# Performance work log

Hardware: AMD Instinct MI355X
Metric: run time of the kernel (lower is better)

The kernel has to match this reference:

```python
import jax, jax.numpy as jnp
import numpy as np
import math

B, S, D, H, L, FF = 16, 512, 1024, 16, 4, 4096
DK = D // H
EPS = 1e-5
NEG = -1e32


def make_pe(max_len, d_model):
    pos = np.arange(max_len, dtype=np.float32)[:, None]
    div = np.exp(np.arange(0, d_model, 2, dtype=np.float32) * (-math.log(10000.0) / d_model))
    pe = np.zeros((max_len, d_model), dtype=np.float32)
    pe[:, 0::2] = np.sin(pos * div)
    pe[:, 1::2] = np.cos(pos * div)
    return jnp.asarray(pe[None])  # [1, max_len, d_model]


def setup_inputs() -> dict:
    key = jax.random.key(0)
    ks = jax.random.split(key, 32)
    sd = 0.02
    inp = {
        'q_embed_data': jax.random.normal(ks[0], (B, S, D), jnp.float32),
        'qa_embed_data': jax.random.normal(ks[1], (B, S, D), jnp.float32),
        'forget_rate': jax.random.uniform(ks[2], (B, 1, S, 1), jnp.float32),
        'pe': make_pe(S, D),
        'Wk': jax.random.normal(ks[3], (L, D, D), jnp.float32) * sd,
        'bk': jnp.zeros((L, D), jnp.float32),
        'Wv': jax.random.normal(ks[4], (L, D, D), jnp.float32) * sd,
        'bv': jnp.zeros((L, D), jnp.float32),
        'Wo': jax.random.normal(ks[5], (L, D, D), jnp.float32) * sd,
        'bo': jnp.zeros((L, D), jnp.float32),
        'W1': jax.random.normal(ks[6], (L, D, FF), jnp.float32) * sd,
        'b1': jnp.zeros((L, FF), jnp.float32),
        'W2': jax.random.normal(ks[7], (L, FF, D), jnp.float32) * sd,
        'b2': jnp.zeros((L, D), jnp.float32),
        'ln1_g': jnp.ones((L, D), jnp.float32),
        'ln1_b': jnp.zeros((L, D), jnp.float32),
        'ln2_g': jnp.ones((L, D), jnp.float32),
        'ln2_b': jnp.zeros((L, D), jnp.float32),
    }
    return inp


def layernorm(x, g, b):
    m = jnp.mean(x, -1, keepdims=True)
    v = jnp.mean((x - m) ** 2, -1, keepdims=True)
    return (x - m) * jax.lax.rsqrt(v + EPS) * g + b


def forward(q_embed_data, qa_embed_data, forget_rate, pe,
            Wk, bk, Wv, bv, Wo, bo, W1, b1, W2, b2,
            ln1_g, ln1_b, ln2_g, ln2_b):
    x = q_embed_data + pe[:, :S]
    y = qa_embed_data + pe[:, :S]
    # mask==0 path: allowed positions are strictly below diagonal (j < i)
    allowed = jnp.tril(jnp.ones((S, S), bool), k=-1)
    scale = 1.0 / math.sqrt(DK)
    for l in range(L):
        # kq_same: q also uses k_linear
        k = (x @ Wk[l] + bk[l]).reshape(B, S, H, DK).transpose(0, 2, 1, 3)
        q = k
        v = (y @ Wv[l] + bv[l]).reshape(B, S, H, DK).transpose(0, 2, 1, 3)
        scores = jnp.einsum('bhid,bhjd->bhij', q, k) * scale
        scores = scores * forget_rate  # [B,1,S,1] broadcasts over heads/cols
        scores = jnp.where(allowed, scores, NEG)
        attn = jax.nn.softmax(scores, axis=-1)
        attn = attn.at[:, :, 0, :].set(0.0)  # zero_pad of first query row
        out = jnp.einsum('bhij,bhjd->bhid', attn, v)
        out = out.transpose(0, 2, 1, 3).reshape(B, S, D) @ Wo[l] + bo[l]
        x = layernorm(x + out, ln1_g[l], ln1_b[l])
        ff = jax.nn.relu(x @ W1[l] + b1[l]) @ W2[l] + b2[l]
        x = layernorm(x + ff, ln2_g[l], ln2_b[l])
    return x


def reference(q_embed_data, qa_embed_data, forget_rate, pe,
              Wk, bk, Wv, bv, Wo, bo, W1, b1, W2, b2,
              ln1_g, ln1_b, ln2_g, ln2_b):
    return forward(q_embed_data, qa_embed_data, forget_rate, pe,
                   Wk, bk, Wv, bv, Wo, bo, W1, b1, W2, b2,
                   ln1_g, ln1_b, ln2_g, ln2_b)
```

## Files before the change

### kernel.cpp

```cpp
#include <hip/hip_runtime.h>
#include <hip/hip_bf16.h>
#include <cstdint>
#include <cstddef>

#define Bq 16
#define Sq 512
#define Dq 1024
#define Hq 16
#define Lq 4
#define FFq 4096
#define Mq (Bq * Sq)

typedef unsigned short ushort_t;
typedef __attribute__((ext_vector_type(8))) short short8;
typedef __attribute__((ext_vector_type(8))) unsigned short ushortx8;
typedef __attribute__((ext_vector_type(4))) unsigned short ushortx4;
typedef __attribute__((ext_vector_type(4))) float floatx4;

__device__ __forceinline__ float bf2f(ushort_t u) {
  union { unsigned int i; float f; } x;
  x.i = ((unsigned int)u) << 16;
  return x.f;
}
__device__ __forceinline__ ushort_t f2bf(float f) {
  unsigned int u = __float_as_uint(f);
  u += 0x7fffu + ((u >> 16) & 1u);
  return (ushort_t)(u >> 16);
}

#define GLL16(gp, lp) __builtin_amdgcn_global_load_lds( \
    (__attribute__((address_space(1))) void*)(gp),      \
    (__attribute__((address_space(3))) void*)(lp), 16, 0, 0)

__global__ void probe_kernel(const ushort_t* __restrict__ pe,
                             const ushort_t* __restrict__ g1,
                             int* __restrict__ flags)
{
  if (threadIdx.x == 0 && blockIdx.x == 0) {
    flags[0] = (pe[1] == (ushort_t)0x3F80u) ? 1 : 0;
    flags[1] = (g1[0] == (ushort_t)0x3F80u) ? 1 : 0;
  }
}

struct CvtArgs {
  const void* src[10];
  ushort_t*   dst[10];
  int         n[10];
  int         fi[10];
  int         cum[11];
};
__global__ __launch_bounds__(256) void convert_all_kernel(
    CvtArgs a, const int* __restrict__ flags)
{
  const int bidx = blockIdx.x;
  int s = 0;
  while (s < 9 && bidx >= a.cum[s + 1]) ++s;
  const int i = (bidx - a.cum[s]) * 256 + threadIdx.x;
  if (i >= a.n[s]) return;
  if (flags[a.fi[s]]) a.dst[s][i] = ((const ushort_t*)a.src[s])[i];
  else                a.dst[s][i] = f2bf(((const float*)a.src[s])[i]);
}

__global__ __launch_bounds__(256) void gemm_bt_kernel(
    const ushort_t* __restrict__ A, const ushort_t* __restrict__ BT,
    const ushort_t* __restrict__ bias, ushort_t* __restrict__ C,
    int N, int K, int relu)
{
  __shared__ __align__(16) ushort_t As[2][128 * 32];
  __shared__ __align__(16) ushort_t Bs[2][128 * 32];

  const int t = threadIdx.x;
  const int lane = t & 63;
  const int w = t >> 6;
  const int la = lane & 15;
  const int lb = lane >> 4;

  int bx = blockIdx.x, by = blockIdx.y;
  {
    const int gx = gridDim.x, gy = gridDim.y;
    if ((gy & 7) == 0) {
      const int orig = by * gx + bx;
      const int xcd = orig & 7;
      const int local = orig >> 3;
      const int rows = gy >> 3;
      const int mi = local % rows;
      const int ni = local / rows;
      by = xcd * rows + mi;
      bx = ni;
    }
  }
  const long m0 = (long)by * 128;
  const long n0 = (long)bx * 128;
  const int nk = K >> 5;

  const int r0 = t >> 2;
  const int c0 = (t & 3) << 3;
  const ushort_t* gA = A + (m0 + r0) * K + c0;
  const ushort_t* gB = BT + (n0 + r0) * K + c0;
  const long rowoff = (long)64 * K;
  const int lo0 = (w * 64) * 8;
  const int lo1 = (w * 64 + 256) * 8;

  const floatx4 z4 = {0.f, 0.f, 0.f, 0.f};
  floatx4 acc[4][4];
#pragma unroll
  for (int i = 0; i < 4; ++i)
#pragma unroll
    for (int j = 0; j < 4; ++j) acc[i][j] = z4;

  GLL16(gA, &As[0][lo0]);
  GLL16(gA + rowoff, &As[0][lo1]);
  GLL16(gB, &Bs[0][lo0]);
  GLL16(gB + rowoff, &Bs[0][lo1]);
  __syncthreads();

  const int wm = (w >> 1) * 64;
  const int wn = (w & 1) * 64;
  int cur = 0;

  for (int kt = 1; kt < nk; ++kt) {
    const long ko = (long)kt * 32;
    GLL16(gA + ko, &As[cur ^ 1][lo0]);
    GLL16(gA + rowoff + ko, &As[cur ^ 1][lo1]);
    GLL16(gB + ko, &Bs[cur ^ 1][lo0]);
    GLL16(gB + rowoff + ko, &Bs[cur ^ 1][lo1]);

    short8 af[4], bfr[4];
#pragma unroll
    for (int mf = 0; mf < 4; ++mf)
      af[mf] = *(const short8*)&As[cur][(wm + mf * 16 + la) * 32 + lb * 8];
#pragma unroll
    for (int nf = 0; nf < 4; ++nf)
      bfr[nf] = *(const short8*)&Bs[cur][(wn + nf * 16 + la) * 32 + lb * 8];
#pragma unroll
    for (int mf = 0; mf < 4; ++mf)
#pragma unroll
      for (int nf = 0; nf < 4; ++nf)
        acc[mf][nf] = __builtin_amdgcn_mfma_f32_16x16x32_bf16(af[mf], bfr[nf], acc[mf][nf], 0, 0, 0);

    __syncthreads();
    cur ^= 1;
  }
  {
    short8 af[4], bfr[4];
#pragma unroll
    for (int mf = 0; mf < 4; ++mf)
      af[mf] = *(const short8*)&As[cur][(wm + mf * 16 + la) * 32 + lb * 8];
#pragma unroll
    for (int nf = 0; nf < 4; ++nf)
      bfr[nf] = *(const short8*)&Bs[cur][(wn + nf * 16 + la) * 32 + lb * 8];
#pragma unroll
    for (int mf = 0; mf < 4; ++mf)
#pragma unroll
      for (int nf = 0; nf < 4; ++nf)
        acc[mf][nf] = __builtin_amdgcn_mfma_f32_16x16x32_bf16(af[mf], bfr[nf], acc[mf][nf], 0, 0, 0);
  }

#pragma unroll
  for (int nf = 0; nf < 4; ++nf) {
    const long col = n0 + wn + nf * 16 + la;
    const float bsv = bf2f(bias[col]);
#pragma unroll
    for (int mf = 0; mf < 4; ++mf) {
      const long row = m0 + wm + mf * 16 + lb * 4;
      ushort_t* cp = C + row * N + col;
      const floatx4 v = acc[mf][nf];
#pragma unroll
      for (int r = 0; r < 4; ++r) {
        float x = v[r] + bsv;
        if (relu) x = fmaxf(x, 0.0f);
        cp[(long)r * N] = f2bf(x);
      }
    }
  }
}

__global__ __launch_bounds__(256) void attn_kernel(
    const ushort_t* __restrict__ kq, const ushort_t* __restrict__ vt,
    const ushort_t* __restrict__ fr, ushort_t* __restrict__ ao)
{
  __shared__ __align__(16) ushort_t P[4][64 * 72];
  const int t = threadIdx.x;
  const int lane = t & 63;
  const int w4 = t >> 6;
  const int wq = blockIdx.y * 4 + w4;
  const int b = blockIdx.x >> 4;
  const int h = blockIdx.x & 15;
  const int la = lane & 15;
  const int lb = lane >> 4;
  const int i0 = wq * 64;
  const long kbase = ((long)b * Sq) * Dq + h * 64;
  const long vbase = ((long)(b * Hq + h)) * (64L * Sq);

  short8 qf[4][2];
#pragma unroll
  for (int mf = 0; mf < 4; ++mf)
#pragma unroll
    for (int tt = 0; tt < 2; ++tt)
      qf[mf][tt] = *(const short8*)&kq[kbase + (long)(i0 + mf * 16 + la) * Dq + tt * 32 + lb * 8];

  float frs[4][4];
#pragma unroll
  for (int mf = 0; mf < 4; ++mf)
#pragma unroll
    for (int r = 0; r < 4; ++r)
      frs[mf][r] = 0.125f * bf2f(fr[b * Sq + i0 + mf * 16 + lb * 4 + r]);

  const floatx4 z4 = {0.f, 0.f, 0.f, 0.f};
  floatx4 o[4][4];
  float mrun[4][4], lrun[4][4];
#pragma unroll
  for (int mf = 0; mf < 4; ++mf)
#pragma unroll
    for (int x = 0; x < 4; ++x) {
      o[mf][x] = z4;
      mrun[mf][x] = -1e30f;
      lrun[mf][x] = 0.0f;
    }

  for (int jt = 0; jt <= wq; ++jt) {
    const int j0 = jt * 64;
    floatx4 s[4][4];
#pragma unroll
    for (int mf = 0; mf < 4; ++mf)
#pragma unroll
      for (int jf = 0; jf < 4; ++jf) s[mf][jf] = z4;

#pragma unroll
    for (int tt = 0; tt < 2; ++tt) {
      short8 kf[4];
#pragma unroll
      for (int jf = 0; jf < 4; ++jf)
        kf[jf] = *(const short8*)&kq[kbase + (long)(j0 + jf * 16 + la) * Dq + tt * 32 + lb * 8];
#pragma unroll
      for (int mf = 0; mf < 4; ++mf)
#pragma unroll
        for (int jf = 0; jf < 4; ++jf)
          s[mf][jf] = __builtin_amdgcn_mfma_f32_16x16x32_bf16(qf[mf][tt], kf[jf], s[mf][jf], 0, 0, 0);
    }

    const bool diag = (jt == wq);
#pragma unroll
    for (int mf = 0; mf < 4; ++mf)
#pragma unroll
      for (int jf = 0; jf < 4; ++jf)
#pragma unroll
        for (int r = 0; r < 4; ++r) {
          float x = s[mf][jf][r] * frs[mf][r];
          if (diag && (j0 + jf * 16 + la) >= (i0 + mf * 16 + lb * 4 + r)) x = -1e30f;
          s[mf][jf][r] = x;
        }

#pragma unroll
    for (int mf = 0; mf < 4; ++mf)
#pragma unroll
      for (int r = 0; r < 4; ++r) {
        float pm = fmaxf(fmaxf(s[mf][0][r], s[mf][1][r]), fmaxf(s[mf][2][r], s[mf][3][r]));
        pm = fmaxf(pm, __shfl_xor(pm, 1));
        pm = fmaxf(pm, __shfl_xor(pm, 2));
        pm = fmaxf(pm, __shfl_xor(pm, 4));
        pm = fmaxf(pm, __shfl_xor(pm, 8));
        const float mo = mrun[mf][r];
        const float mn = fmaxf(mo, pm);
        const float sc = __expf(mo - mn);
        mrun[mf][r] = mn;
        float rs = 0.0f;
#pragma unroll
        for (int jf = 0; jf < 4; ++jf) {
          const float p = __expf(s[mf][jf][r] - mn);
          s[mf][jf][r] = p;
          rs += p;
        }
        rs += __shfl_xor(rs, 1);
        rs += __shfl_xor(rs, 2);
        rs += __shfl_xor(rs, 4);
        rs += __shfl_xor(rs, 8);
        lrun[mf][r] = lrun[mf][r] * sc + rs;
#pragma unroll
        for (int df = 0; df < 4; ++df) o[mf][df][r] *= sc;
      }

#pragma unroll
    for (int mf = 0; mf < 4; ++mf)
#pragma unroll
      for (int jf = 0; jf < 4; ++jf)
#pragma unroll
        for (int r = 0; r < 4; ++r)
          P[w4][(mf * 16 + lb * 4 + r) * 72 + jf * 16 + la] = f2bf(s[mf][jf][r]);

#pragma unroll
    for (int tt = 0; tt < 2; ++tt) {
      short8 pf[4], vf[4];
#pragma unroll
      for (int mf = 0; mf < 4; ++mf)
        pf[mf] = *(const short8*)&P[w4][(mf * 16 + la) * 72 + tt * 32 + lb * 8];
#pragma unroll
      for (int df = 0; df < 4; ++df)
        vf[df] = *(const short8*)&vt[vbase + (long)(df * 16 + la) * Sq + j0 + tt * 32 + lb * 8];
#pragma unroll
      for (int mf = 0; mf < 4; ++mf)
#pragma unroll
        for (int df = 0; df < 4; ++df)
          o[mf][df] = __builtin_amdgcn_mfma_f32_16x16x32_bf16(pf[mf], vf[df], o[mf][df], 0, 0, 0);
    }
  }

#pragma unroll
  for (int mf = 0; mf < 4; ++mf)
#pragma unroll
    for (int df = 0; df < 4; ++df)
#pragma unroll
      for (int r = 0; r < 4; ++r) {
        const int ii = i0 + mf * 16 + lb * 4 + r;
        const float vv = (ii == 0) ? 0.0f : o[mf][df][r] / lrun[mf][r];
        ao[((long)b * Sq + ii) * Dq + h * 64 + df * 16 + la] = f2bf(vv);
      }
}

__global__ __launch_bounds__(256) void ln_kernel(
    float* __restrict__ xf, const ushort_t* __restrict__ add,
    const ushort_t* __restrict__ g, const ushort_t* __restrict__ bb,
    ushort_t* __restrict__ outb, float* __restrict__ outf,
    const int* __restrict__ flags, int final_)
{
  __shared__ float red[2][4];
  const long row = blockIdx.x;
  const int t = threadIdx.x;
  const int c = t * 4;
  float* xr = xf + row * Dq;
  const ushort_t* ar = add + row * Dq;

  floatx4 xv = *(floatx4*)&xr[c];
  ushortx4 av = *(const ushortx4*)&ar[c];
  float v[4];
  float s1 = 0.f, s2 = 0.f;
#pragma unroll
  for (int e = 0; e < 4; ++e) {
    v[e] = xv[e] + bf2f(av[e]);
    s1 += v[e];
    s2 += v[e] * v[e];
  }
#pragma unroll
  for (int m = 1; m < 64; m <<= 1) {
    s1 += __shfl_xor(s1, m);
    s2 += __shfl_xor(s2, m);
  }
  const int lane = t & 63, w = t >> 6;
  if (lane == 0) { red[0][w] = s1; red[1][w] = s2; }
  __syncthreads();
  s1 = red[0][0] + red[0][1] + red[0][2] + red[0][3];
  s2 = red[1][0] + red[1][1] + red[1][2] + red[1][3];
  const float mean = s1 * (1.0f / Dq);
  const float var = fmaxf(s2 * (1.0f / Dq) - mean * mean, 0.0f);
  const float rstd = rsqrtf(var + 1e-5f);
  ushortx4 gv = *(const ushortx4*)&g[c];
  ushortx4 bv = *(const ushortx4*)&bb[c];
  ushortx4 ob;
  floatx4 xo;
#pragma unroll
  for (int e = 0; e < 4; ++e) {
    const float y = (v[e] - mean) * rstd * bf2f(gv[e]) + bf2f(bv[e]);
    xo[e] = y;
    ob[e] = f2bf(y);
  }
  *(floatx4*)&xr[c] = xo;
  if (final_ && !flags[0]) {
    *(floatx4*)&outf[row * Dq + c] = xo;
  } else {
    *(ushortx4*)&outb[row * Dq + c] = ob;
  }
}

__global__ __launch_bounds__(256) void addpe_kernel(
    const void* __restrict__ qe, const void* __restrict__ qa,
    const void* __restrict__ pe, float* __restrict__ xf,
    ushort_t* __restrict__ xb, ushort_t* __restrict__ yb,
    const int* __restrict__ flags)
{
  const long i = ((long)blockIdx.x * 256 + threadIdx.x) * 8;
  const long sd = i & ((long)Sq * Dq - 1);
  const bool isb = flags[0] != 0;
  float q[8], a[8], p[8];
  if (isb) {
    ushortx8 q8 = *(const ushortx8*)((const ushort_t*)qe + i);
    ushortx8 a8 = *(const ushortx8*)((const ushort_t*)qa + i);
    ushortx8 p8 = *(const ushortx8*)((const ushort_t*)pe + sd);
#pragma unroll
    for (int e = 0; e < 8; ++e) { q[e] = bf2f(q8[e]); a[e] = bf2f(a8[e]); p[e] = bf2f(p8[e]); }
  } else {
    const float* qp = (const float*)qe + i;
    const float* ap = (const float*)qa + i;
    const float* pp = (const float*)pe + sd;
    floatx4 q0 = *(const floatx4*)qp, q1 = *(const floatx4*)(qp + 4);
    floatx4 a0 = *(const floatx4*)ap, a1 = *(const floatx4*)(ap + 4);
    floatx4 p0 = *(const floatx4*)pp, p1 = *(const floatx4*)(pp + 4);
#pragma unroll
    for (int e = 0; e < 4; ++e) {
      q[e] = q0[e]; q[e + 4] = q1[e];
      a[e] = a0[e]; a[e + 4] = a1[e];
      p[e] = p0[e]; p[e + 4] = p1[e];
    }
  }
  ushortx8 xo, yo;
  floatx4 f0, f1;
#pragma unroll
  for (int e = 0; e < 8; ++e) {
    const float xvv = (isb ? q[e] : bf2f(f2bf(q[e]))) + (isb ? p[e] : bf2f(f2bf(p[e])));
    const float yvv = (isb ? a[e] : bf2f(f2bf(a[e]))) + (isb ? p[e] : bf2f(f2bf(p[e])));
    if (e < 4) { f0[e] = xvv; } else { f1[e - 4] = xvv; }
    xo[e] = f2bf(xvv);
    yo[e] = f2bf(yvv);
  }
  *(floatx4*)&xf[i] = f0;
  *(floatx4*)&xf[i + 4] = f1;
  *(ushortx8*)&xb[i] = xo;
  *(ushortx8*)&yb[i] = yo;
}

__global__ __launch_bounds__(256) void transpose_kernel(
    const void* __restrict__ src, ushort_t* __restrict__ dst, int K, int N,
    const int* __restrict__ flags)
{
  __shared__ __align__(16) ushort_t tile[64][72];
  const bool isb = flags[1] != 0;
  const long base = (long)blockIdx.z * K * N;
  const int k0 = blockIdx.y * 64, n0 = blockIdx.x * 64;
  const int t = threadIdx.x;
  const int r = t >> 3;
  const int cc = (t & 7) << 3;
#pragma unroll
  for (int it = 0; it < 2; ++it) {
    const int rr = r + it * 32;
    const long gi = base + (long)(k0 + rr) * N + n0 + cc;
    if (isb) {
      *(short8*)&tile[rr][cc] = *(const short8*)((const ushort_t*)src + gi);
    } else {
      const float* sf = (const float*)src + gi;
      floatx4 v0 = *(const floatx4*)sf;
      floatx4 v1 = *(const floatx4*)(sf + 4);
#pragma unroll
      for (int e = 0; e < 4; ++e) {
        tile[rr][cc + e] = f2bf(v0[e]);
        tile[rr][cc + 4 + e] = f2bf(v1[e]);
      }
    }
  }
  __syncthreads();
#pragma unroll
  for (int it = 0; it < 2; ++it) {
    const int rr = r + it * 32;
    short8 v;
#pragma unroll
    for (int e = 0; e < 8; ++e) v[e] = (short)tile[cc + e][rr];
    *(short8*)&dst[base + (long)(n0 + rr) * K + k0 + cc] = v;
  }
}

__global__ __launch_bounds__(256) void vtrans_kernel(
    const ushort_t* __restrict__ vb, ushort_t* __restrict__ vt)
{
  __shared__ __align__(16) ushort_t tile[64][72];
  const int b = blockIdx.y >> 4, h = blockIdx.y & 15;
  const int j0 = blockIdx.x * 64;
  const int t = threadIdx.x;
  const int r = t >> 3;
  const int cc = (t & 7) << 3;
#pragma unroll
  for (int it = 0; it < 2; ++it) {
    const int rr = r + it * 32;
    *(short8*)&tile[rr][cc] = *(const short8*)&vb[((long)b * Sq + j0 + rr) * Dq + h * 64 + cc];
  }
  __syncthreads();
#pragma unroll
  for (int it = 0; it < 2; ++it) {
    const int rr = r + it * 32;
    short8 v;
#pragma unroll
    for (int e = 0; e < 8; ++e) v[e] = (short)tile[cc + e][rr];
    *(short8*)&vt[((long)(b * Hq + h) * 64 + rr) * Sq + j0 + cc] = v;
  }
}

extern "C" void kernel_launch(void* const* d_in, const int* in_sizes, int n_in,
                              void* d_out, int out_size, void* d_ws, size_t ws_size,
                              hipStream_t stream)
{
  if (n_in < 18) return;
  const void* qe  = d_in[0];
  const void* qa  = d_in[1];
  const void* fr  = d_in[2];
  const void* pe  = d_in[3];
  const void* Wk  = d_in[4];
  const void* bk  = d_in[5];
  const void* Wv  = d_in[6];
  const void* bv  = d_in[7];
  const void* Wo  = d_in[8];
  const void* bo  = d_in[9];
  const void* W1  = d_in[10];
  const void* b1  = d_in[11];
  const void* W2  = d_in[12];
  const void* b2  = d_in[13];
  const void* g1  = d_in[14];
  const void* be1 = d_in[15];
  const void* g2  = d_in[16];
  const void* be2 = d_in[17];

  char* ws = (char*)d_ws;
  const size_t SM = 243269632L;
  const size_t NEED = SM + 114752L;
  if (ws_size < NEED) return;

  float*    xf   = (float*)   (ws + 0L);
  ushort_t* xb   = (ushort_t*)(ws + 33554432L);
  ushort_t* yb   = (ushort_t*)(ws + 50331648L);
  ushort_t* tmpD = (ushort_t*)(ws + 67108864L);
  ushort_t* WkT  = (ushort_t*)(ws + 83886080L);
  ushort_t* WvT  = (ushort_t*)(ws + 92274688L);
  ushort_t* WoT  = (ushort_t*)(ws + 100663296L);
  ushort_t* W1T  = (ushort_t*)(ws + 109051904L);
  ushort_t* W2T  = (ushort_t*)(ws + 142606336L);
  ushort_t* kb   = (ushort_t*)(ws + 176160768L);
  ushort_t* vbf  = (ushort_t*)(ws + 192937984L);
  ushort_t* vtb  = (ushort_t*)(ws + 209715200L);
  ushort_t* ff1  = kb;

  int*      flags = (int*)(ws + SM);
  ushort_t* frc  = (ushort_t*)(ws + SM + 64);
  ushort_t* bkc  = (ushort_t*)(ws + SM + 16448);
  ushort_t* bvc  = (ushort_t*)(ws + SM + 24640);
  ushort_t* boc  = (ushort_t*)(ws + SM + 32832);
  ushort_t* b1c  = (ushort_t*)(ws + SM + 41024);
  ushort_t* b2c  = (ushort_t*)(ws + SM + 73792);
  ushort_t* g1c  = (ushort_t*)(ws + SM + 81984);
  ushort_t* be1c = (ushort_t*)(ws + SM + 90176);
  ushort_t* g2c  = (ushort_t*)(ws + SM + 98368);
  ushort_t* be2c = (ushort_t*)(ws + SM + 106560);

  probe_kernel<<<1, 64, 0, stream>>>((const ushort_t*)pe, (const ushort_t*)g1, flags);

  {
    CvtArgs a;
    const void* srcs[10] = {fr, bk, bv, bo, b1, b2, g1, be1, g2, be2};
    ushort_t*   dsts[10] = {frc, bkc, bvc, boc, b1c, b2c, g1c, be1c, g2c, be2c};
    const int   ns[10]   = {8192, 4096, 4096, 4096, 16384, 4096, 4096, 4096, 4096, 4096};
    int cum = 0;
    for (int s = 0; s < 10; ++s) {
      a.src[s] = srcs[s]; a.dst[s] = dsts[s]; a.n[s] = ns[s];
      a.fi[s] = (s == 0) ? 0 : 1;
      a.cum[s] = cum;
      cum += (ns[s] + 255) / 256;
    }
    a.cum[10] = cum;
    convert_all_kernel<<<cum, 256, 0, stream>>>(a, flags);
  }

  transpose_kernel<<<dim3(16, 16, 4), 256, 0, stream>>>(Wk, WkT, 1024, 1024, flags);
  transpose_kernel<<<dim3(16, 16, 4), 256, 0, stream>>>(Wv, WvT, 1024, 1024, flags);
  transpose_kernel<<<dim3(16, 16, 4), 256, 0, stream>>>(Wo, WoT, 1024, 1024, flags);
  transpose_kernel<<<dim3(64, 16, 4), 256, 0, stream>>>(W1, W1T, 1024, 4096, flags);
  transpose_kernel<<<dim3(16, 64, 4), 256, 0, stream>>>(W2, W2T, 4096, 1024, flags);

  addpe_kernel<<<4096, 256, 0, stream>>>(qe, qa, pe, xf, xb, yb, flags);

  for (int l = 0; l < 4; ++l) {
    gemm_bt_kernel<<<dim3(8, 64), 256, 0, stream>>>(xb, WkT + (long)l * 1048576, bkc + l * 1024, kb, 1024, 1024, 0);
    gemm_bt_kernel<<<dim3(8, 64), 256, 0, stream>>>(yb, WvT + (long)l * 1048576, bvc + l * 1024, vbf, 1024, 1024, 0);
    vtrans_kernel<<<dim3(8, 256), 256, 0, stream>>>(vbf, vtb);
    attn_kernel<<<dim3(256, 2), 256, 0, stream>>>(kb, vtb, frc, vbf);
    gemm_bt_kernel<<<dim3(8, 64), 256, 0, stream>>>(vbf, WoT + (long)l * 1048576, boc + l * 1024, tmpD, 1024, 1024, 0);
    ln_kernel<<<8192, 256, 0, stream>>>(xf, tmpD, g1c + l * 1024, be1c + l * 1024, xb, nullptr, flags, 0);
    gemm_bt_kernel<<<dim3(32, 64), 256, 0, stream>>>(xb, W1T + (long)l * 4194304, b1c + l * 4096, ff1, 4096, 1024, 1);
    gemm_bt_kernel<<<dim3(8, 64), 256, 0, stream>>>(ff1, W2T + (long)l * 4194304, b2c + l * 1024, tmpD, 1024, 4096, 0);
    if (l == 3) {
      ln_kernel<<<8192, 256, 0, stream>>>(xf, tmpD, g2c + l * 1024, be2c + l * 1024,
                                          (ushort_t*)d_out, (float*)d_out, flags, 1);
    } else {
      ln_kernel<<<8192, 256, 0, stream>>>(xf, tmpD, g2c + l * 1024, be2c + l * 1024,
                                          xb, nullptr, flags, 0);
    }
  }
}
```

Measured before the change: 1.840 ms.

## Deepen GEMM pipeline to four LDS stages with XOR-swizzled layout

The GEMM main loop moves from a double buffer to a four-buffer LDS ring with three tiles prefetched ahead, and uses explicit vmcnt waits so loads for later tiles stay in flight while the current tile is computed. The LDS layout is also XOR-swizzled on the k-chunk index, in both the global-to-LDS placement and the fragment reads, to reduce bank conflicts. LDS use doubles to 64KB per block, which may lower occupancy. Correctness depends on the hand-counted vmcnt values matching the number of outstanding loads.

```diff
diff --git a/kernel.cpp b/kernel.cpp
--- a/kernel.cpp
+++ b/kernel.cpp
@@ -66,8 +66,8 @@
     const ushort_t* __restrict__ bias, ushort_t* __restrict__ C,
     int N, int K, int relu)
 {
-  __shared__ __align__(16) ushort_t As[2][128 * 32];
-  __shared__ __align__(16) ushort_t Bs[2][128 * 32];
+  __shared__ __align__(16) ushort_t As[4][4096];
+  __shared__ __align__(16) ushort_t Bs[4][4096];
 
   const int t = threadIdx.x;
   const int lane = t & 63;
@@ -83,23 +83,25 @@
       const int xcd = orig & 7;
       const int local = orig >> 3;
       const int rows = gy >> 3;
-      const int mi = local % rows;
-      const int ni = local / rows;
-      by = xcd * rows + mi;
-      bx = ni;
+      by = xcd * rows + local % rows;
+      bx = local / rows;
     }
   }
   const long m0 = (long)by * 128;
   const long n0 = (long)bx * 128;
   const int nk = K >> 5;
 
-  const int r0 = t >> 2;
-  const int c0 = (t & 3) << 3;
-  const ushort_t* gA = A + (m0 + r0) * K + c0;
-  const ushort_t* gB = BT + (n0 + r0) * K + c0;
-  const long rowoff = (long)64 * K;
-  const int lo0 = (w * 64) * 8;
-  const int lo1 = (w * 64 + 256) * 8;
+  const int f0 = (w << 7) + lane;
+  const int f1 = f0 + 64;
+  const int rA0 = f0 >> 2, rA1 = f1 >> 2;
+  const int kA0 = ((f0 & 3) ^ ((rA0 >> 1) & 3)) << 3;
+  const int kA1 = ((f1 & 3) ^ ((rA1 >> 1) & 3)) << 3;
+  const ushort_t* gA0 = A + (m0 + rA0) * K + kA0;
+  const ushort_t* gA1 = A + (m0 + rA1) * K + kA1;
+  const ushort_t* gB0 = BT + (n0 + rA0) * K + kA0;
+  const ushort_t* gB1 = BT + (n0 + rA1) * K + kA1;
+  const int lo0 = (w * 2 + 0) * 512;
+  const int lo1 = (w * 2 + 1) * 512;
 
   const floatx4 z4 = {0.f, 0.f, 0.f, 0.f};
   floatx4 acc[4][4];
@@ -108,53 +110,51 @@
 #pragma unroll
     for (int j = 0; j < 4; ++j) acc[i][j] = z4;
 
-  GLL16(gA, &As[0][lo0]);
-  GLL16(gA + rowoff, &As[0][lo1]);
-  GLL16(gB, &Bs[0][lo0]);
-  GLL16(gB + rowoff, &Bs[0][lo1]);
-  __syncthreads();
+#define STAGE(buf, kt) do {                      \
+    const long ko_ = (long)(kt) << 5;            \
+    GLL16(gA0 + ko_, &As[(buf)][lo0]);           \
+    GLL16(gA1 + ko_, &As[(buf)][lo1]);           \
+    GLL16(gB0 + ko_, &Bs[(buf)][lo0]);           \
+    GLL16(gB1 + ko_, &Bs[(buf)][lo1]);           \
+  } while (0)
+
+  STAGE(0, 0);
+  STAGE(1, 1);
+  STAGE(2, 2);
 
   const int wm = (w >> 1) * 64;
   const int wn = (w & 1) * 64;
-  int cur = 0;
-
-  for (int kt = 1; kt < nk; ++kt) {
-    const long ko = (long)kt * 32;
-    GLL16(gA + ko, &As[cur ^ 1][lo0]);
-    GLL16(gA + rowoff + ko, &As[cur ^ 1][lo1]);
-    GLL16(gB + ko, &Bs[cur ^ 1][lo0]);
-    GLL16(gB + rowoff + ko, &Bs[cur ^ 1][lo1]);
-
+
+  for (int kt = 0; kt < nk; ++kt) {
+    const int rem = nk - 1 - kt;
+    if (rem >= 2)      asm volatile("s_waitcnt vmcnt(8)" ::: "memory");
+    else if (rem == 1) asm volatile("s_waitcnt vmcnt(4)" ::: "memory");
+    else               asm volatile("s_waitcnt vmcnt(0)" ::: "memory");
+    __builtin_amdgcn_s_barrier();
+
+    const int cur = kt & 3;
     short8 af[4], bfr[4];
 #pragma unroll
-    for (int mf = 0; mf < 4; ++mf)
-      af[mf] = *(const short8*)&As[cur][(wm + mf * 16 + la) * 32 + lb * 8];
-#pragma unroll
-    for (int nf = 0; nf < 4; ++nf)
-      bfr[nf] = *(const short8*)&Bs[cur][(wn + nf * 16 + la) * 32 + lb * 8];
+    for (int mf = 0; mf < 4; ++mf) {
+      const int r = wm + mf * 16 + la;
+      af[mf] = *(const short8*)&As[cur][r * 32 + ((lb ^ ((r >> 1) & 3)) << 3)];
+    }
+#pragma unroll
+    for (int nf = 0; nf < 4; ++nf) {
+      const int r = wn + nf * 16 + la;
+      bfr[nf] = *(const short8*)&Bs[cur][r * 32 + ((lb ^ ((r >> 1) & 3)) << 3)];
+    }
 #pragma unroll
     for (int mf = 0; mf < 4; ++mf)
 #pragma unroll
       for (int nf = 0; nf < 4; ++nf)
         acc[mf][nf] = __builtin_amdgcn_mfma_f32_16x16x32_bf16(af[mf], bfr[nf], acc[mf][nf], 0, 0, 0);
 
-    __syncthreads();
-    cur ^= 1;
-  }
-  {
-    short8 af[4], bfr[4];
-#pragma unroll
-    for (int mf = 0; mf < 4; ++mf)
-      af[mf] = *(const short8*)&As[cur][(wm + mf * 16 + la) * 32 + lb * 8];
-#pragma unroll
-    for (int nf = 0; nf < 4; ++nf)
-      bfr[nf] = *(const short8*)&Bs[cur][(wn + nf * 16 + la) * 32 + lb * 8];
-#pragma unroll
-    for (int mf = 0; mf < 4; ++mf)
-#pragma unroll
-      for (int nf = 0; nf < 4; ++nf)
-        acc[mf][nf] = __builtin_amdgcn_mfma_f32_16x16x32_bf16(af[mf], bfr[nf], acc[mf][nf], 0, 0, 0);
-  }
+    asm volatile("s_waitcnt lgkmcnt(0)" ::: "memory");
+    __builtin_amdgcn_s_barrier();
+    if (kt + 3 < nk) STAGE((kt + 3) & 3, kt + 3);
+  }
+#undef STAGE
 
 #pragma unroll
   for (int nf = 0; nf < 4; ++nf) {
```

After: 1.879 ms. +2.2%, slower.
